# Kernel optimization log

Hardware: AMD Instinct MI355X
Metric: run time of the kernel (lower is better)

The kernel has to match this reference:

```python
import jax, jax.numpy as jnp
import numpy as np
import math

B, S, H, DK, NB = 2, 128, 4, 128, 4
D = H * DK  # 512


def setup_inputs() -> dict:
    key = jax.random.key(0)
    ks = jax.random.split(key, 24)
    g = lambda i, sh, std=1.0: jax.random.normal(ks[i], sh, jnp.float32) * std
    u = lambda i, sh: jax.random.uniform(ks[i], sh, jnp.float32)
    return {
        "x_m": g(0, (B, S, D)), "x_c": g(1, (B, S, D)),
        "b_m": g(2, (B, S, D)), "b_c": g(3, (B, S, D)),
        "bb_m": g(4, (B, NB, NB, D)), "bb_c": u(5, (B, NB, NB, D)),
        "p_m": g(6, (B, S, D)), "p_c": u(7, (B, S, D)),
        "W_xm": g(8, (3, D, H, DK), 0.02), "W_xc": g(9, (3, D, H, DK), 0.02),
        "W_bm": g(10, (3, D, H, DK), 0.02), "W_bc": g(11, (3, D, H, DK), 0.02),
        "Wq1_w": g(12, (DK, DK), 0.05), "Wq1_b": g(13, (DK,), 0.02),
        "Wq2_w": g(14, (DK, DK), 0.05), "Wq2_b": g(15, (DK,), 0.02),
        "Wk1_w": g(16, (DK, DK), 0.05), "Wk1_b": g(17, (DK,), 0.02),
        "Wk2_w": g(18, (DK, DK), 0.05), "Wk2_b": g(19, (DK,), 0.02),
        "mean_w": g(20, (D, D), 0.02), "mean_b": jnp.zeros((D,), jnp.float32),
        "cov_w": g(21, (D, D), 0.02), "cov_b": jnp.zeros((D,), jnp.float32),
        "ln_w": jnp.ones((D,), jnp.float32), "ln_b": jnp.zeros((D,), jnp.float32),
        "b_seq": jax.random.randint(ks[22], (B, S), 0, NB),
    }


def _elu1(x):
    return jax.nn.elu(x) + 1.0


def _tri_sagp(m1, m2, m3, c1, c2, c3):
    # fuse three diagonal Gaussians by product-of-Gaussians (precision-weighted)
    eps = 1e-24
    p1 = 1.0 / jnp.clip(c1, eps)
    p2 = 1.0 / jnp.clip(c2, eps)
    p3 = 1.0 / jnp.clip(c3, eps)
    c = 1.0 / (p1 + p2 + p3)
    return c * (m1 * p1 + m2 * p2 + m3 * p3), c


def _ln(x, w, b):
    m = jnp.mean(x, -1, keepdims=True)
    v = jnp.mean((x - m) ** 2, -1, keepdims=True)
    return (x - m) / jnp.sqrt(v + 1e-12) * w + b


def _forward(x_m, x_c, b_m, b_c, bb_m, bb_c, p_m, p_c,
             W_xm, W_xc, W_bm, W_bc,
             Wq1_w, Wq1_b, Wq2_w, Wq2_b, Wk1_w, Wk1_b, Wk2_w, Wk2_b,
             mean_w, mean_b, cov_w, cov_b, ln_w, ln_b, b_seq):
    Bb, Ss, Dd = x_m.shape
    Hh, Dk = W_xm.shape[2], W_xm.shape[3]
    proj = lambda x, w: jnp.einsum('bnd,dhk->bhnk', x, w)
    q1 = proj(x_m, W_xm[0]) + proj(b_m, W_bm[0])
    k1 = proj(x_m, W_xm[1]) + proj(b_m, W_bm[1])
    v1 = proj(x_m, W_xm[2]) + proj(b_m, W_bm[2])
    q2 = _elu1(proj(x_c, W_xc[0]) + proj(b_c, W_bc[0]))
    k2 = _elu1(proj(x_c, W_xc[1]) + proj(b_c, W_bc[1]))
    v2 = _elu1(proj(x_c, W_xc[2]) + proj(b_c, W_bc[2]))
    nb = bb_m.shape[1]
    # [B,NB,NB,D] -> [B,H,NB,NB,DK]
    bbm = bb_m.reshape(Bb, nb, nb, Hh, Dk).transpose(0, 3, 1, 2, 4)
    bbc = bb_c.reshape(Bb, nb, nb, Hh, Dk).transpose(0, 3, 1, 2, 4)
    # out[b,h,i,j,:] = bbm[b,h,b_seq[b,j],b_seq[b,i],:]  (matches torch advanced indexing + permute)
    gather = jax.vmap(lambda bb, seq: bb[:, seq[None, :], seq[:, None], :])
    bbm_b = gather(bbm, b_seq)  # [B,H,S,S,DK]
    bbc_b = gather(bbc, b_seq)
    pm = p_m.reshape(Bb, Ss, Hh, Dk).transpose(0, 2, 1, 3)  # [B,H,S,DK]
    pc = p_c.reshape(Bb, Ss, Hh, Dk).transpose(0, 2, 1, 3)
    lin = lambda x, w, b: x @ w.T + b
    fQm, fQc = _tri_sagp(q1[:, :, :, None, :], lin(bbm_b, Wq1_w, Wq1_b),
                         lin(pm, Wq2_w, Wq2_b)[:, :, :, None, :],
                         q2[:, :, :, None, :], bbc_b, pc[:, :, :, None, :])
    fKm, fKc = _tri_sagp(k1[:, :, None, :, :], lin(bbm_b, Wk1_w, Wk1_b),
                         lin(pm, Wk2_w, Wk2_b)[:, :, None, :, :],
                         k2[:, :, None, :, :], bbc_b, pc[:, :, None, :, :])
    eps = 1e-24
    # 2-Wasserstein^2 between diagonal Gaussians (the 1x1 matmul form reduces to this)
    w2 = jnp.sum((fQm - fKm) ** 2, -1) + jnp.sum(
        (jnp.sqrt(jnp.clip(fQc, eps)) - jnp.sqrt(jnp.clip(fKc, eps))) ** 2, -1)
    scores = -w2 / math.sqrt(Dk)  # [B,H,S,S]
    probs = jax.nn.softmax(scores, axis=-1)
    mean_ctx = jnp.einsum('bhij,bhjk->bhik', probs, v1)
    cov_ctx = jnp.einsum('bhij,bhjk->bhik', probs ** 2, v2)
    mean_ctx = mean_ctx.transpose(0, 2, 1, 3).reshape(Bb, Ss, Dd)
    cov_ctx = cov_ctx.transpose(0, 2, 1, 3).reshape(Bb, Ss, Dd)
    mean_h = _ln(mean_ctx @ mean_w.T + mean_b + x_m, ln_w, ln_b)
    cov_h = _ln(cov_ctx @ cov_w.T + cov_b + x_c, ln_w, ln_b)
    return mean_h, cov_h, probs


def reference(x_m, x_c, b_m, b_c, bb_m, bb_c, p_m, p_c,
              W_xm, W_xc, W_bm, W_bc,
              Wq1_w, Wq1_b, Wq2_w, Wq2_b, Wk1_w, Wk1_b, Wk2_w, Wk2_b,
              mean_w, mean_b, cov_w, cov_b, ln_w, ln_b, b_seq):
    return _forward(x_m, x_c, b_m, b_c, bb_m, bb_c, p_m, p_c,
                    W_xm, W_xc, W_bm, W_bc,
                    Wq1_w, Wq1_b, Wq2_w, Wq2_b, Wk1_w, Wk1_b, Wk2_w, Wk2_b,
                    mean_w, mean_b, cov_w, cov_b, ln_w, ln_b, b_seq)
```

## Files before the change

### kernel.cpp

```cpp
#include <hip/hip_runtime.h>
#include <math.h>

#define B_ 2
#define S_ 128
#define H_ 4
#define DK_ 128
#define NB_ 4
#define D_ 512
#define M_ 256

typedef __attribute__((ext_vector_type(8))) short short8;
typedef __attribute__((ext_vector_type(4))) float float4v;
typedef __attribute__((ext_vector_type(4))) unsigned short ushort4v;

__device__ __forceinline__ float elu1(float x) {
    return (x > 0.f) ? (x + 1.f) : __expf(x);
}

__device__ __forceinline__ unsigned short f2bf(float f) {
    unsigned u = __float_as_uint(f);
    unsigned r = (u + 0x7FFFu + ((u >> 16) & 1u)) >> 16;
    return (unsigned short)r;
}


__global__ __launch_bounds__(256) void k_prep(
    const float* __restrict__ x_m, const float* __restrict__ b_m,
    const float* __restrict__ x_c, const float* __restrict__ b_c,
    const float* __restrict__ mean_w, const float* __restrict__ cov_w,
    const float* __restrict__ W_xm, const float* __restrict__ W_xc,
    const float* __restrict__ W_bm, const float* __restrict__ W_bc,
    const float* __restrict__ p_m, const float* __restrict__ bb_m,
    const float* __restrict__ Wq2, const float* __restrict__ Wk2,
    const float* __restrict__ Wq1, const float* __restrict__ Wk1,
    unsigned short* __restrict__ A_m, unsigned short* __restrict__ A_c,
    unsigned short* __restrict__ wm_bf, unsigned short* __restrict__ wc_bf,
    unsigned short* __restrict__ Wt,
    unsigned short* __restrict__ pm_bf, unsigned short* __restrict__ bbm_bf,
    unsigned short* __restrict__ w4_bf)
{
    __shared__ unsigned short tile[32][33];
    const int t = threadIdx.x;
    const int blk = blockIdx.x;
    const int NBK = gridDim.x;

    for (int cid = blk * 256 + t; cid < 315392; cid += NBK * 256) {
        const float* srcp;
        unsigned short* dstp;
        if (cid < 262144) {
            int job = cid >> 16;
            int off = (cid & 65535) * 4;
            if (job <= 1) {
                int m = off >> 10, k = off & 1023;
                if (job == 0) { srcp = (k < 512) ? (x_m + m * 512 + k) : (b_m + m * 512 + k - 512); dstp = A_m + off; }
                else          { srcp = (k < 512) ? (x_c + m * 512 + k) : (b_c + m * 512 + k - 512); dstp = A_c + off; }
            } else if (job == 2) { srcp = mean_w + off; dstp = wm_bf + off; }
            else                 { srcp = cov_w + off;  dstp = wc_bf + off; }
        } else if (cid < 294912) {
            int off = (cid - 262144) * 4;
            srcp = p_m + off; dstp = pm_bf + off;
        } else if (cid < 299008) {
            int off = (cid - 294912) * 4;
            srcp = bb_m + off; dstp = bbm_bf + off;
        } else {
            int off = (cid - 299008) * 4;
            int seg = off >> 14;
            const float* Ws = (seg == 0) ? Wq2 : (seg == 1) ? Wk2 : (seg == 2) ? Wq1 : Wk1;
            srcp = Ws + (off & 16383); dstp = w4_bf + off;
        }
        float4 v = *(const float4*)srcp;
        ushort4v o4;
        o4.x = f2bf(v.x); o4.y = f2bf(v.y); o4.z = f2bf(v.z); o4.w = f2bf(v.w);
        *(ushort4v*)dstp = o4;
    }

    const int tx = t & 31, ty = t >> 5;
    for (int tid = blk; tid < 3072; tid += NBK) {
        int nt = tid & 15, kt = (tid >> 4) & 15, z = tid >> 8;
        int o = z >> 1, part = z & 1;
        const float* src;
        if (part == 0) src = (o < 3) ? (W_xm + o * 262144) : (W_xc + (o - 3) * 262144);
        else           src = (o < 3) ? (W_bm + o * 262144) : (W_bc + (o - 3) * 262144);
        __syncthreads();
#pragma unroll
        for (int u = 0; u < 4; ++u)
            tile[ty + u * 8][tx] = f2bf(src[(kt * 32 + ty + u * 8) * 512 + nt * 32 + tx]);
        __syncthreads();
        unsigned short* dst = Wt + o * 524288 + part * 512;
#pragma unroll
        for (int u = 0; u < 4; ++u)
            dst[(nt * 32 + ty + u * 8) * 1024 + kt * 32 + tx] = tile[tx][ty + u * 8];
    }
}

__global__ __launch_bounds__(256) void k_mm(
    const unsigned short* __restrict__ A_m, const unsigned short* __restrict__ A_c,
    const unsigned short* __restrict__ Wt,
    const unsigned short* __restrict__ pm_bf, const unsigned short* __restrict__ bbm_bf,
    const unsigned short* __restrict__ w4_bf,
    const float* __restrict__ bq2, const float* __restrict__ bk2,
    const float* __restrict__ bq1, const float* __restrict__ bk1,
    float* __restrict__ qkv, float* __restrict__ pq, float* __restrict__ pk,
    float* __restrict__ bbq, float* __restrict__ bbk)
{
    const int t = threadIdx.x;
    const int wid = blockIdx.x * 4 + (t >> 6);
    const int lane = t & 63;
    const int l15 = lane & 15, quad = lane >> 4;

    if (wid < 3072) {
        const int o = wid >> 9;
        const int rem = wid & 511;
        const int nt = rem & 31, mt = rem >> 5;
        const int m0 = mt * 16, n0 = nt * 16;

        const unsigned short* A = (o < 3) ? A_m : A_c;
        const unsigned short* ap = A + (m0 + l15) * 1024 + quad * 8;
        const unsigned short* bp = Wt + o * 524288 + (n0 + l15) * 1024 + quad * 8;

        float4v acc0 = {0.f, 0.f, 0.f, 0.f};
        float4v acc1 = {0.f, 0.f, 0.f, 0.f};
#pragma unroll
        for (int k0 = 0; k0 < 1024; k0 += 64) {
            short8 a0 = *(const short8*)(ap + k0);
            short8 b0 = *(const short8*)(bp + k0);
            short8 a1 = *(const short8*)(ap + k0 + 32);
            short8 b1 = *(const short8*)(bp + k0 + 32);
            acc0 = __builtin_amdgcn_mfma_f32_16x16x32_bf16(a0, b0, acc0, 0, 0, 0);
            acc1 = __builtin_amdgcn_mfma_f32_16x16x32_bf16(a1, b1, acc1, 0, 0, 0);
        }
        float* dst = qkv + o * 131072;
#pragma unroll
        for (int r = 0; r < 4; ++r) {
            float v = acc0[r] + acc1[r];
            if (o >= 3) v = elu1(v);
            dst[(m0 + quad * 4 + r) * 512 + n0 + l15] = v;
        }
    } else {
        const unsigned short* Abf;
        const unsigned short* Wb;
        const float* bias;
        float* dst;
        int m0, n0, h;
        if (wid < 4096) {
            int lid = wid - 3072;
            int sel = lid >> 9;
            int r = lid & 511;
            h = r >> 7;
            int rem = r & 127;
            m0 = (rem >> 3) * 16; n0 = (rem & 7) * 16;
            Abf = pm_bf;
            Wb = w4_bf + sel * 16384;
            bias = sel ? bk2 : bq2;
            dst = sel ? pk : pq;
        } else {
            int lid = wid - 4096;
            int sel = lid >> 6;
            int r = lid & 63;
            h = r >> 4;
            int rem = r & 15;
            m0 = (rem >> 3) * 16; n0 = (rem & 7) * 16;
            Abf = bbm_bf;
            Wb = w4_bf + 32768 + sel * 16384;
            bias = sel ? bk1 : bq1;
            dst = sel ? bbk : bbq;
        }
        const unsigned short* ap = Abf + (m0 + l15) * 512 + h * 128 + quad * 8;
        const unsigned short* bp = Wb + (n0 + l15) * 128 + quad * 8;

        float4v acc0 = {0.f, 0.f, 0.f, 0.f};
        float4v acc1 = {0.f, 0.f, 0.f, 0.f};
#pragma unroll
        for (int k0 = 0; k0 < 128; k0 += 64) {
            short8 a0 = *(const short8*)(ap + k0);
            short8 b0 = *(const short8*)(bp + k0);
            short8 a1 = *(const short8*)(ap + k0 + 32);
            short8 b1 = *(const short8*)(bp + k0 + 32);
            acc0 = __builtin_amdgcn_mfma_f32_16x16x32_bf16(a0, b0, acc0, 0, 0, 0);
            acc1 = __builtin_amdgcn_mfma_f32_16x16x32_bf16(a1, b1, acc1, 0, 0, 0);
        }
        float bv = bias[n0 + l15];
#pragma unroll
        for (int r = 0; r < 4; ++r)
            dst[(m0 + quad * 4 + r) * 512 + h * 128 + n0 + l15] = acc0[r] + acc1[r] + bv;
    }
}

__global__ __launch_bounds__(128) void k_fuseK(
    const float* __restrict__ qkv, const float* __restrict__ pk,
    const float* __restrict__ bbk, const float* __restrict__ bb_c,
    const float* __restrict__ p_c, const int* __restrict__ b_seq,
    float* __restrict__ fKm, float* __restrict__ fKs)
{
    const int t = threadIdx.x;
    const int j = blockIdx.x, h = blockIdx.y, b = blockIdx.z;
    const int d = h * 128 + t;
    const float eps = 1e-24f;
    const int base = (b * S_ + j) * D_ + d;
    const int sj = b_seq[b * S_ + j];

    float m1 = qkv[M_ * D_ + base];
    float c1 = qkv[4 * M_ * D_ + base];
    float m3 = pk[base];
    float c3 = p_c[base];

    float p1 = 1.f / fmaxf(c1, eps);
    float p3 = 1.f / fmaxf(c3, eps);
    float mp13 = m1 * p1 + m3 * p3;

#pragma unroll
    for (int sv = 0; sv < 4; ++sv) {
        int idx = (b * 16 + sj * 4 + sv) * 512 + d;
        float m2 = bbk[idx];
        float c2 = bb_c[idx];
        float p2 = 1.f / fmaxf(c2, eps);
        float cc = 1.f / (p1 + p2 + p3);
        int o = (((b * H_ + h) * 4 + sv) * S_ + j) * 128 + t;
        fKm[o] = cc * (mp13 + m2 * p2);
        fKs[o] = sqrtf(fmaxf(cc, eps));
    }
}

__global__ __launch_bounds__(128) void k_attn3(
    const float* __restrict__ qkv, const float* __restrict__ pq,
    const float* __restrict__ bbq, const float* __restrict__ bb_c,
    const float* __restrict__ p_c, const int* __restrict__ b_seq,
    const float* __restrict__ fKm, const float* __restrict__ fKs,
    float* __restrict__ probs_out, unsigned short* __restrict__ mctxb,
    unsigned short* __restrict__ cctxb)
{
    const int t = threadIdx.x;
    const int i = blockIdx.x, h = blockIdx.y, b = blockIdx.z;
    const float eps = 1e-24f;

    __shared__ __attribute__((aligned(16))) float qm[4 * 132];
    __shared__ __attribute__((aligned(16))) float qs[4 * 132];
    __shared__ float red[4];
    __shared__ float pr[128], pr2[128];

    const int si = b_seq[b * S_ + i];
    const int sj = b_seq[b * S_ + t];

    {
        const int d = h * 128 + t;
        const int base = (b * S_ + i) * D_ + d;
        float m1 = qkv[base];
        float c1 = qkv[3 * M_ * D_ + base];
        float m3 = pq[base];
        float c3 = p_c[base];
        float p1 = 1.f / fmaxf(c1, eps);
        float p3 = 1.f / fmaxf(c3, eps);
        float mp13 = m1 * p1 + m3 * p3;
#pragma unroll
        for (int sv = 0; sv < 4; ++sv) {
            int idx = (b * 16 + sv * 4 + si) * 512 + d;
            float m2 = bbq[idx];
            float c2 = bb_c[idx];
            float p2 = 1.f / fmaxf(c2, eps);
            float cc = 1.f / (p1 + p2 + p3);
            qm[sv * 132 + t] = cc * (mp13 + m2 * p2);
            qs[sv * 132 + t] = sqrtf(fmaxf(cc, eps));
        }
    }
    __syncthreads();

    const int krow = (((b * H_ + h) * 4 + si) * S_ + t) * 128;
    const float4* kmp = (const float4*)(fKm + krow);
    const float4* ksp = (const float4*)(fKs + krow);

    float w2 = 0.f;
#pragma unroll 4
    for (int k4 = 0; k4 < 32; ++k4) {
        float4 km = kmp[k4];
        float4 ks = ksp[k4];
        float4 m = *(const float4*)&qm[sj * 132 + k4 * 4];
        float4 s = *(const float4*)&qs[sj * 132 + k4 * 4];
        float d0 = m.x - km.x, d1 = m.y - km.y, d2 = m.z - km.z, d3 = m.w - km.w;
        float e0 = s.x - ks.x, e1 = s.y - ks.y, e2 = s.z - ks.z, e3 = s.w - ks.w;
        w2 += d0 * d0 + d1 * d1 + d2 * d2 + d3 * d3
            + e0 * e0 + e1 * e1 + e2 * e2 + e3 * e3;
    }
    float score = -w2 * 0.08838834764831845f;

    float mx = score;
#pragma unroll
    for (int off = 32; off >= 1; off >>= 1) mx = fmaxf(mx, __shfl_xor(mx, off));
    if ((t & 63) == 0) red[t >> 6] = mx;
    __syncthreads();
    mx = fmaxf(red[0], red[1]);
    float e = __expf(score - mx);
    float sm = e;
#pragma unroll
    for (int off = 32; off >= 1; off >>= 1) sm += __shfl_xor(sm, off);
    if ((t & 63) == 0) red[2 + (t >> 6)] = sm;
    __syncthreads();
    float p = e / (red[2] + red[3]);

    probs_out[((b * H_ + h) * S_ + i) * S_ + t] = p;
    pr[t] = p;
    pr2[t] = p * p;
    __syncthreads();

    const float* v1 = qkv + 2 * M_ * D_ + (b * S_) * D_ + h * 128 + t;
    const float* v2 = qkv + 5 * M_ * D_ + (b * S_) * D_ + h * 128 + t;
    float am = 0.f, ac = 0.f;
#pragma unroll 8
    for (int j = 0; j < 128; ++j) {
        am = fmaf(pr[j], v1[j * D_], am);
        ac = fmaf(pr2[j], v2[j * D_], ac);
    }
    mctxb[(b * S_ + i) * D_ + h * 128 + t] = f2bf(am);
    cctxb[(b * S_ + i) * D_ + h * 128 + t] = f2bf(ac);
}

__global__ __launch_bounds__(256) void k_fin_mm(
    const unsigned short* __restrict__ mctxb, const unsigned short* __restrict__ cctxb,
    const unsigned short* __restrict__ wm_bf, const unsigned short* __restrict__ wc_bf,
    float* __restrict__ y_m, float* __restrict__ y_c)
{
    const int t = threadIdx.x;
    const int wid = blockIdx.x * 4 + (t >> 6);
    const int lane = t & 63;
    const int mat = wid >> 9;
    const int rem = wid & 511;
    const int nt = rem & 31, mt = rem >> 5;
    const int m0 = mt * 16, n0 = nt * 16;
    const int l15 = lane & 15, quad = lane >> 4;

    const unsigned short* A = mat ? cctxb : mctxb;
    const unsigned short* Bw = mat ? wc_bf : wm_bf;
    float* y = mat ? y_c : y_m;

    const unsigned short* ap = A + (m0 + l15) * 512 + quad * 8;
    const unsigned short* bp = Bw + (n0 + l15) * 512 + quad * 8;

    float4v acc0 = {0.f, 0.f, 0.f, 0.f};
    float4v acc1 = {0.f, 0.f, 0.f, 0.f};
#pragma unroll
    for (int k0 = 0; k0 < 512; k0 += 64) {
        short8 a0 = *(const short8*)(ap + k0);
        short8 b0 = *(const short8*)(bp + k0);
        short8 a1 = *(const short8*)(ap + k0 + 32);
        short8 b1 = *(const short8*)(bp + k0 + 32);
        acc0 = __builtin_amdgcn_mfma_f32_16x16x32_bf16(a0, b0, acc0, 0, 0, 0);
        acc1 = __builtin_amdgcn_mfma_f32_16x16x32_bf16(a1, b1, acc1, 0, 0, 0);
    }
#pragma unroll
    for (int r = 0; r < 4; ++r)
        y[(m0 + quad * 4 + r) * 512 + n0 + l15] = acc0[r] + acc1[r];
}

__global__ __launch_bounds__(256) void k_ln(
    const float* __restrict__ y_m, const float* __restrict__ y_c,
    const float* __restrict__ mean_b, const float* __restrict__ cov_b,
    const float* __restrict__ x_m, const float* __restrict__ x_c,
    const float* __restrict__ ln_w, const float* __restrict__ ln_b,
    float* __restrict__ out)
{
    const int t = threadIdx.x;
    const int id = blockIdx.x;
    const int mat = id >> 8, row = id & 255;
    const float* yg = mat ? y_c : y_m;
    const float* bias = mat ? cov_b : mean_b;
    const float* res = mat ? x_c : x_m;
    const int base = row * 512;

    __shared__ float red[8];

    float y0 = yg[base + t] + bias[t] + res[base + t];
    float y1 = yg[base + 256 + t] + bias[256 + t] + res[base + 256 + t];
    float s = y0 + y1, ss = y0 * y0 + y1 * y1;
#pragma unroll
    for (int off = 32; off >= 1; off >>= 1) { s += __shfl_xor(s, off); ss += __shfl_xor(ss, off); }
    if ((t & 63) == 0) { red[t >> 6] = s; red[4 + (t >> 6)] = ss; }
    __syncthreads();
    float mu = (red[0] + red[1] + red[2] + red[3]) * (1.f / 512.f);
    float var = (red[4] + red[5] + red[6] + red[7]) * (1.f / 512.f) - mu * mu;
    float rstd = 1.f / sqrtf(var + 1e-12f);
    out[mat * 131072 + base + t] = (y0 - mu) * rstd * ln_w[t] + ln_b[t];
    out[mat * 131072 + base + 256 + t] = (y1 - mu) * rstd * ln_w[256 + t] + ln_b[256 + t];
}

extern "C" void kernel_launch(void* const* d_in, const int* in_sizes, int n_in,
                              void* d_out, int out_size, void* d_ws, size_t ws_size,
                              hipStream_t stream) {
    (void)in_sizes; (void)n_in; (void)out_size; (void)ws_size;
    const float* x_m   = (const float*)d_in[0];
    const float* x_c   = (const float*)d_in[1];
    const float* b_m   = (const float*)d_in[2];
    const float* b_c   = (const float*)d_in[3];
    const float* bb_m  = (const float*)d_in[4];
    const float* bb_c  = (const float*)d_in[5];
    const float* p_m   = (const float*)d_in[6];
    const float* p_c   = (const float*)d_in[7];
    const float* W_xm  = (const float*)d_in[8];
    const float* W_xc  = (const float*)d_in[9];
    const float* W_bm  = (const float*)d_in[10];
    const float* W_bc  = (const float*)d_in[11];
    const float* Wq1_w = (const float*)d_in[12];
    const float* Wq1_b = (const float*)d_in[13];
    const float* Wq2_w = (const float*)d_in[14];
    const float* Wq2_b = (const float*)d_in[15];
    const float* Wk1_w = (const float*)d_in[16];
    const float* Wk1_b = (const float*)d_in[17];
    const float* Wk2_w = (const float*)d_in[18];
    const float* Wk2_b = (const float*)d_in[19];
    const float* mean_w = (const float*)d_in[20];
    const float* mean_b = (const float*)d_in[21];
    const float* cov_w  = (const float*)d_in[22];
    const float* cov_b  = (const float*)d_in[23];
    const float* ln_w   = (const float*)d_in[24];
    const float* ln_b   = (const float*)d_in[25];
    const int*   b_seq  = (const int*)d_in[26];

    float* ws = (float*)d_ws;
    float* qkv = ws;
    float* pq  = ws + 786432;
    float* pk  = ws + 917504;
    float* bbq = ws + 1048576;
    float* bbk = ws + 1064960;
    float* fKm = ws + 1081344;
    float* fKs = ws + 1605632;
    float* y_m = ws + 2129920;
    float* y_c = ws + 2260992;
    unsigned short* A_m    = (unsigned short*)(ws + 2392064);
    unsigned short* A_c    = (unsigned short*)(ws + 2523136);
    unsigned short* Wt     = (unsigned short*)(ws + 2654208);
    unsigned short* wm_bf  = (unsigned short*)(ws + 4227072);
    unsigned short* wc_bf  = (unsigned short*)(ws + 4358144);
    unsigned short* mctxb  = (unsigned short*)(ws + 4489216);
    unsigned short* cctxb  = (unsigned short*)(ws + 4554752);
    unsigned short* pm_bf  = (unsigned short*)(ws + 4620288);
    unsigned short* bbm_bf = (unsigned short*)(ws + 4685824);
    unsigned short* w4_bf  = (unsigned short*)(ws + 4694016);
    float* out = (float*)d_out;

    k_prep<<<dim3(768), 256, 0, stream>>>(
        x_m, b_m, x_c, b_c, mean_w, cov_w, W_xm, W_xc, W_bm, W_bc,
        p_m, bb_m, Wq2_w, Wk2_w, Wq1_w, Wk1_w,
        A_m, A_c, wm_bf, wc_bf, Wt, pm_bf, bbm_bf, w4_bf);
    k_mm<<<dim3(1056), 256, 0, stream>>>(
        A_m, A_c, Wt, pm_bf, bbm_bf, w4_bf,
        Wq2_b, Wk2_b, Wq1_b, Wk1_b,
        qkv, pq, pk, bbq, bbk);
    k_fuseK<<<dim3(128, 4, 2), 128, 0, stream>>>(
        qkv, pk, bbk, bb_c, p_c, b_seq, fKm, fKs);
    k_attn3<<<dim3(128, 4, 2), 128, 0, stream>>>(
        qkv, pq, bbq, bb_c, p_c, b_seq, fKm, fKs, out + 262144, mctxb, cctxb);
    k_fin_mm<<<dim3(256), 256, 0, stream>>>(
        mctxb, cctxb, wm_bf, wc_bf, y_m, y_c);
    k_ln<<<dim3(512), 256, 0, stream>>>(
        y_m, y_c, mean_b, cov_b, x_m, x_c, ln_w, ln_b, out);
}
```

Measured before the change: 177.5 us.

## Fuse output projection GEMM with residual add and LayerNorm into one kernel

Replaces the separate output-projection MFMA kernel and LayerNorm kernel with one kernel. Each block computes a 16-row strip of the full 512-wide output into shared memory, then applies bias, residual and LayerNorm in place. This removes a kernel launch and the global round-trip of the intermediate y buffers. In exchange the grid shrinks from 256 to 32 blocks, and each wave serially computes 8 output tiles, which cuts parallelism.

```diff
diff --git a/kernel.cpp b/kernel.cpp
--- a/kernel.cpp
+++ b/kernel.cpp
@@ -313,72 +313,74 @@
     cctxb[(b * S_ + i) * D_ + h * 128 + t] = f2bf(ac);
 }
 
-__global__ __launch_bounds__(256) void k_fin_mm(
+__global__ __launch_bounds__(256) void k_fin(
     const unsigned short* __restrict__ mctxb, const unsigned short* __restrict__ cctxb,
     const unsigned short* __restrict__ wm_bf, const unsigned short* __restrict__ wc_bf,
-    float* __restrict__ y_m, float* __restrict__ y_c)
-{
-    const int t = threadIdx.x;
-    const int wid = blockIdx.x * 4 + (t >> 6);
-    const int lane = t & 63;
-    const int mat = wid >> 9;
-    const int rem = wid & 511;
-    const int nt = rem & 31, mt = rem >> 5;
-    const int m0 = mt * 16, n0 = nt * 16;
-    const int l15 = lane & 15, quad = lane >> 4;
-
-    const unsigned short* A = mat ? cctxb : mctxb;
-    const unsigned short* Bw = mat ? wc_bf : wm_bf;
-    float* y = mat ? y_c : y_m;
-
-    const unsigned short* ap = A + (m0 + l15) * 512 + quad * 8;
-    const unsigned short* bp = Bw + (n0 + l15) * 512 + quad * 8;
-
-    float4v acc0 = {0.f, 0.f, 0.f, 0.f};
-    float4v acc1 = {0.f, 0.f, 0.f, 0.f};
-#pragma unroll
-    for (int k0 = 0; k0 < 512; k0 += 64) {
-        short8 a0 = *(const short8*)(ap + k0);
-        short8 b0 = *(const short8*)(bp + k0);
-        short8 a1 = *(const short8*)(ap + k0 + 32);
-        short8 b1 = *(const short8*)(bp + k0 + 32);
-        acc0 = __builtin_amdgcn_mfma_f32_16x16x32_bf16(a0, b0, acc0, 0, 0, 0);
-        acc1 = __builtin_amdgcn_mfma_f32_16x16x32_bf16(a1, b1, acc1, 0, 0, 0);
-    }
-#pragma unroll
-    for (int r = 0; r < 4; ++r)
-        y[(m0 + quad * 4 + r) * 512 + n0 + l15] = acc0[r] + acc1[r];
-}
-
-__global__ __launch_bounds__(256) void k_ln(
-    const float* __restrict__ y_m, const float* __restrict__ y_c,
     const float* __restrict__ mean_b, const float* __restrict__ cov_b,
     const float* __restrict__ x_m, const float* __restrict__ x_c,
     const float* __restrict__ ln_w, const float* __restrict__ ln_b,
     float* __restrict__ out)
 {
+    const int mat = blockIdx.x >> 4, mt = blockIdx.x & 15;
+    const int m0 = mt * 16;
+    const unsigned short* A = mat ? cctxb : mctxb;
+    const unsigned short* Bw = mat ? wc_bf : wm_bf;
+
+    __shared__ float y[16][516];
+
     const int t = threadIdx.x;
-    const int id = blockIdx.x;
-    const int mat = id >> 8, row = id & 255;
-    const float* yg = mat ? y_c : y_m;
+    const int wv = t >> 6, lane = t & 63;
+    const int l15 = lane & 15, quad = lane >> 4;
+
+    const unsigned short* ap = A + (m0 + l15) * 512 + quad * 8;
+#pragma unroll
+    for (int u = 0; u < 8; ++u) {
+        int n0 = (wv * 8 + u) * 16;
+        const unsigned short* bp = Bw + (n0 + l15) * 512 + quad * 8;
+        float4v acc0 = {0.f, 0.f, 0.f, 0.f};
+        float4v acc1 = {0.f, 0.f, 0.f, 0.f};
+#pragma unroll
+        for (int k0 = 0; k0 < 512; k0 += 64) {
+            short8 a0 = *(const short8*)(ap + k0);
+            short8 b0 = *(const short8*)(bp + k0);
+            short8 a1 = *(const short8*)(ap + k0 + 32);
+            short8 b1 = *(const short8*)(bp + k0 + 32);
+            acc0 = __builtin_amdgcn_mfma_f32_16x16x32_bf16(a0, b0, acc0, 0, 0, 0);
+            acc1 = __builtin_amdgcn_mfma_f32_16x16x32_bf16(a1, b1, acc1, 0, 0, 0);
+        }
+#pragma unroll
+        for (int r = 0; r < 4; ++r)
+            y[quad * 4 + r][n0 + l15] = acc0[r] + acc1[r];
+    }
+    __syncthreads();
+
+    const int r = t >> 4, c = t & 15;
+    const int row = m0 + r;
     const float* bias = mat ? cov_b : mean_b;
     const float* res = mat ? x_c : x_m;
-    const int base = row * 512;
-
-    __shared__ float red[8];
-
-    float y0 = yg[base + t] + bias[t] + res[base + t];
-    float y1 = yg[base + 256 + t] + bias[256 + t] + res[base + 256 + t];
-    float s = y0 + y1, ss = y0 * y0 + y1 * y1;
-#pragma unroll
-    for (int off = 32; off >= 1; off >>= 1) { s += __shfl_xor(s, off); ss += __shfl_xor(ss, off); }
-    if ((t & 63) == 0) { red[t >> 6] = s; red[4 + (t >> 6)] = ss; }
-    __syncthreads();
-    float mu = (red[0] + red[1] + red[2] + red[3]) * (1.f / 512.f);
-    float var = (red[4] + red[5] + red[6] + red[7]) * (1.f / 512.f) - mu * mu;
+
+    float vals[32];
+    float s = 0.f, ss = 0.f;
+#pragma unroll
+    for (int u = 0; u < 32; ++u) {
+        int col = c + 16 * u;
+        float v = y[r][col] + bias[col] + res[row * 512 + col];
+        vals[u] = v;
+        s += v; ss += v * v;
+    }
+#pragma unroll
+    for (int off = 8; off >= 1; off >>= 1) {
+        s += __shfl_xor(s, off);
+        ss += __shfl_xor(ss, off);
+    }
+    float mu = s * (1.f / 512.f);
+    float var = ss * (1.f / 512.f) - mu * mu;
     float rstd = 1.f / sqrtf(var + 1e-12f);
-    out[mat * 131072 + base + t] = (y0 - mu) * rstd * ln_w[t] + ln_b[t];
-    out[mat * 131072 + base + 256 + t] = (y1 - mu) * rstd * ln_w[256 + t] + ln_b[256 + t];
+#pragma unroll
+    for (int u = 0; u < 32; ++u) {
+        int col = c + 16 * u;
+        out[mat * 131072 + row * 512 + col] = (vals[u] - mu) * rstd * ln_w[col] + ln_b[col];
+    }
 }
 
 extern "C" void kernel_launch(void* const* d_in, const int* in_sizes, int n_in,
@@ -421,8 +423,6 @@
     float* bbk = ws + 1064960;
     float* fKm = ws + 1081344;
     float* fKs = ws + 1605632;
-    float* y_m = ws + 2129920;
-    float* y_c = ws + 2260992;
     unsigned short* A_m    = (unsigned short*)(ws + 2392064);
     unsigned short* A_c    = (unsigned short*)(ws + 2523136);
     unsigned short* Wt     = (unsigned short*)(ws + 2654208);
@@ -447,8 +447,6 @@
         qkv, pk, bbk, bb_c, p_c, b_seq, fKm, fKs);
     k_attn3<<<dim3(128, 4, 2), 128, 0, stream>>>(
         qkv, pq, bbq, bb_c, p_c, b_seq, fKm, fKs, out + 262144, mctxb, cctxb);
-    k_fin_mm<<<dim3(256), 256, 0, stream>>>(
-        mctxb, cctxb, wm_bf, wc_bf, y_m, y_c);
-    k_ln<<<dim3(512), 256, 0, stream>>>(
-        y_m, y_c, mean_b, cov_b, x_m, x_c, ln_w, ln_b, out);
-}
+    k_fin<<<dim3(32), 256, 0, stream>>>(
+        mctxb, cctxb, wm_bf, wc_bf, mean_b, cov_b, x_m, x_c, ln_w, ln_b, out);
+}
```

Measured after the change: 206.4 us. 16.3% more time.
